# Kernel optimization log

Measured on AMD Instinct MI355X. Metric: run time of the kernel, lower is better.

The kernel has to match this reference:

```python
import jax, jax.numpy as jnp
import numpy as np
import math

B, S, D = 4, 2048, 1024
H, DK, DV = 16, 64, 64

def setup_inputs() -> dict:
    key = jax.random.key(0)
    ks = jax.random.split(key, 8)
    query = jax.random.normal(ks[0], (B, S, D), dtype=jnp.float32)
    key_t = jax.random.normal(ks[1], (B, S, D), dtype=jnp.float32)
    value = jax.random.normal(ks[2], (B, S, D), dtype=jnp.float32)
    # causal mask: True = masked (filled with -inf), broadcast over [B,H,S,S]
    mask = jnp.triu(jnp.ones((S, S), dtype=bool), k=1)[None, None, :, :]
    s = 0.02
    w_q = jax.random.normal(ks[3], (D, H * DK), dtype=jnp.float32) * s
    w_k = jax.random.normal(ks[4], (D, H * DK), dtype=jnp.float32) * s
    w_v = jax.random.normal(ks[5], (D, H * DV), dtype=jnp.float32) * s
    w_o = jax.random.normal(ks[6], (H * DV, D), dtype=jnp.float32) * s
    return {"query": query, "key": key_t, "value": value, "mask": mask,
            "w_q": w_q, "w_k": w_k, "w_v": w_v, "w_o": w_o}

def reference(query, key, value, mask, w_q, w_k, w_v, w_o):
    b, s, _ = query.shape
    # projections -> [B, H, S, dk/dv]
    q = (query @ w_q).reshape(b, s, H, DK).transpose(0, 2, 1, 3)
    k = (key @ w_k).reshape(b, s, H, DK).transpose(0, 2, 1, 3)
    v = (value @ w_v).reshape(b, s, H, DV).transpose(0, 2, 1, 3)
    scores = jnp.einsum('bhqd,bhkd->bhqk', q, k) / math.sqrt(DK)
    scores = jnp.where(mask, -jnp.inf, scores)
    attn = jax.nn.softmax(scores, axis=-1)
    out = jnp.einsum('bhqk,bhkd->bhqd', attn, v)
    out = out.transpose(0, 2, 1, 3).reshape(b, s, H * DV)
    return out @ w_o
```

## Files before the change

### kernel.cpp

```cpp
#include <hip/hip_runtime.h>
#include <hip/hip_bf16.h>

#define S_LEN 2048
#define NH 16
#define DHEAD 64
#define DMODEL 1024
#define BATCH 4

typedef __attribute__((ext_vector_type(4))) float f32x4;
typedef __attribute__((ext_vector_type(8))) short bf16x8;
typedef __attribute__((ext_vector_type(4))) short s16x4;
typedef __attribute__((ext_vector_type(4))) float fl4;
typedef __attribute__((ext_vector_type(4))) unsigned u32x4;
typedef __attribute__((ext_vector_type(2))) unsigned u32x2;

static __device__ __forceinline__ short f2bf(float f) {
  unsigned u = __builtin_bit_cast(unsigned, f);
  u += 0x7fffu + ((u >> 16) & 1u);
  return (short)(u >> 16);
}
static __device__ __forceinline__ f32x4 mfma16(bf16x8 a, bf16x8 b, f32x4 c) {
  return __builtin_amdgcn_mfma_f32_16x16x32_bf16(a, b, c, 0, 0, 0);
}
static __device__ __forceinline__ void gl_lds16(const short* g, short* l) {
  __builtin_amdgcn_global_load_lds(
      (const __attribute__((address_space(1))) unsigned*)g,
      (__attribute__((address_space(3))) unsigned*)l, 16, 0, 0);
}
static __device__ __forceinline__ unsigned cvt_pk_bf16(float lo, float hi) {
  unsigned r;
  asm("v_cvt_pk_bf16_f32 %0, %1, %2" : "=v"(r) : "v"(lo), "v"(hi));
  return r;
}

__global__ __launch_bounds__(256) void transpose_w3(
    const float* __restrict__ w0, const float* __restrict__ w1,
    const float* __restrict__ w2, short* __restrict__ o0,
    short* __restrict__ o1, short* __restrict__ o2) {
  const float* W = blockIdx.z == 0 ? w0 : blockIdx.z == 1 ? w1 : w2;
  short* O = blockIdx.z == 0 ? o0 : blockIdx.z == 1 ? o1 : o2;
  __shared__ __align__(16) short T[64][72];
  const int tid = threadIdx.x;
  const int k0 = blockIdx.y * 64, n0 = blockIdx.x * 64;
#pragma unroll
  for (int i = 0; i < 4; ++i) {
    int c = tid + i * 256;
    int kk = c >> 4, nn = (c & 15) << 2;
    fl4 v = *(const fl4*)(W + (size_t)(k0 + kk) * DMODEL + n0 + nn);
    T[nn + 0][kk] = f2bf(v.x);
    T[nn + 1][kk] = f2bf(v.y);
    T[nn + 2][kk] = f2bf(v.z);
    T[nn + 3][kk] = f2bf(v.w);
  }
  __syncthreads();
#pragma unroll
  for (int i = 0; i < 4; ++i) {
    int c = tid + i * 256;
    int nn = c >> 4, kk = (c & 15) << 2;
    *(s16x4*)(O + (size_t)(n0 + nn) * DMODEL + k0 + kk) = *(const s16x4*)&T[nn][kk];
  }
}

__global__ __launch_bounds__(256) void transpose_w1(
    const float* __restrict__ W, short* __restrict__ O) {
  __shared__ __align__(16) short T[64][72];
  const int tid = threadIdx.x;
  const int k0 = blockIdx.y * 64, n0 = blockIdx.x * 64;
#pragma unroll
  for (int i = 0; i < 4; ++i) {
    int c = tid + i * 256;
    int kk = c >> 4, nn = (c & 15) << 2;
    fl4 v = *(const fl4*)(W + (size_t)(k0 + kk) * DMODEL + n0 + nn);
    T[nn + 0][kk] = f2bf(v.x);
    T[nn + 1][kk] = f2bf(v.y);
    T[nn + 2][kk] = f2bf(v.z);
    T[nn + 3][kk] = f2bf(v.w);
  }
  __syncthreads();
#pragma unroll
  for (int i = 0; i < 4; ++i) {
    int c = tid + i * 256;
    int nn = c >> 4, kk = (c & 15) << 2;
    *(s16x4*)(O + (size_t)(n0 + nn) * DMODEL + k0 + kk) = *(const s16x4*)&T[nn][kk];
  }
}

__global__ __launch_bounds__(256) void gemm_qkv(
    const float* __restrict__ q, const float* __restrict__ k,
    const float* __restrict__ v, const short* __restrict__ Wtq,
    const short* __restrict__ Wtk, const short* __restrict__ Wtv,
    short* __restrict__ Qp, short* __restrict__ Kp, short* __restrict__ Vt,
    float qscale) {
  __shared__ __align__(16) short As[128 * 64];
  __shared__ __align__(16) short Bs[128 * 64];
  const int id = blockIdx.x;
  const int z = id >> 9;
  const int l = id & 511;
  const int cx = l & 7, j = l >> 3;
  const int n0 = (j & 7) * 128;
  const int m0 = (cx * 8 + (j >> 3)) * 128;

  const float* Af = z == 0 ? q : z == 1 ? k : v;
  const short* Bt = z == 0 ? Wtq : z == 1 ? Wtk : Wtv;
  short* Out = z == 0 ? Qp : z == 1 ? Kp : Vt;
  const float scale = z == 0 ? qscale : 1.0f;

  const int tid = threadIdx.x, lane = tid & 63, wid = tid >> 6;
  const int wm = (wid >> 1) * 64, wn = (wid & 1) * 64;
  const int lr = lane & 15, g = lane >> 4;

  f32x4 acc[4][4] = {};

  const int baseRow = tid >> 3;
  const int colOff = (((tid & 7) ^ (baseRow & 7)) << 3);
  const int slot0 = g ^ (lr & 7);

  fl4 av[8];
#pragma unroll
  for (int i = 0; i < 8; ++i) {
    const int c = tid + i * 256;
    av[i] = *(const fl4*)(Af + (size_t)(m0 + (c >> 4)) * DMODEL + ((c & 15) << 2));
  }

  for (int k0 = 0; k0 < DMODEL; k0 += 64) {
    __syncthreads();
#pragma unroll
    for (int i = 0; i < 8; ++i) {
      const int c = tid + i * 256;
      const int row = c >> 4, colc = c & 15;
      u32x2 pk;
      pk.x = cvt_pk_bf16(av[i].x, av[i].y);
      pk.y = cvt_pk_bf16(av[i].z, av[i].w);
      *(u32x2*)&As[row * 64 + (((colc >> 1) ^ (row & 7)) << 3) + ((colc & 1) << 2)] = pk;
    }
#pragma unroll
    for (int i = 0; i < 4; ++i) {
      const short* gb = Bt + (size_t)(n0 + baseRow + i * 32) * DMODEL + k0 + colOff;
      gl_lds16(gb, Bs + (tid + i * 256) * 8);
    }
    __syncthreads();

    if (k0 + 64 < DMODEL) {
#pragma unroll
      for (int i = 0; i < 8; ++i) {
        const int c = tid + i * 256;
        av[i] = *(const fl4*)(Af + (size_t)(m0 + (c >> 4)) * DMODEL + k0 + 64 + ((c & 15) << 2));
      }
    }

#pragma unroll
    for (int ks = 0; ks < 2; ++ks) {
      const int so = (slot0 ^ (ks << 2)) << 3;
      bf16x8 af[4], bfr[4];
#pragma unroll
      for (int t = 0; t < 4; ++t) {
        af[t] = *(const bf16x8*)&As[(wm + t * 16 + lr) * 64 + so];
        bfr[t] = *(const bf16x8*)&Bs[(wn + t * 16 + lr) * 64 + so];
      }
#pragma unroll
      for (int mi = 0; mi < 4; ++mi)
#pragma unroll
        for (int ni = 0; ni < 4; ++ni)
          acc[mi][ni] = mfma16(af[mi], bfr[ni], acc[mi][ni]);
    }
  }

  if (z < 2) {
#pragma unroll
    for (int mi = 0; mi < 4; ++mi)
#pragma unroll
      for (int ni = 0; ni < 4; ++ni) {
        const int n = n0 + wn + ni * 16 + lr;
        const int h = n >> 6, d = n & 63;
#pragma unroll
        for (int r = 0; r < 4; ++r) {
          const int m = m0 + wm + mi * 16 + g * 4 + r;
          const int b = m >> 11, s = m & (S_LEN - 1);
          Out[(((size_t)b * NH + h) * S_LEN + s) * DHEAD + d] =
              f2bf(acc[mi][ni][r] * scale);
        }
      }
  } else {
#pragma unroll
    for (int mi = 0; mi < 4; ++mi) {
      const int mb = m0 + wm + mi * 16 + g * 4;
      const int b = mb >> 11, s = mb & (S_LEN - 1);
#pragma unroll
      for (int ni = 0; ni < 4; ++ni) {
        const int n = n0 + wn + ni * 16 + lr;
        const int h = n >> 6, d = n & 63;
        s16x4 pv;
        pv.x = f2bf(acc[mi][ni][0]);
        pv.y = f2bf(acc[mi][ni][1]);
        pv.z = f2bf(acc[mi][ni][2]);
        pv.w = f2bf(acc[mi][ni][3]);
        *(s16x4*)(Out + (((size_t)b * NH + h) * DHEAD + d) * S_LEN + s) = pv;
      }
    }
  }
}

__global__ __launch_bounds__(256) void gemm_out(
    const short* __restrict__ Ab, const short* __restrict__ Bt,
    float* __restrict__ Out) {
  __shared__ __align__(16) short As[128 * 64];
  __shared__ __align__(16) short Bs[128 * 64];
  const int id = blockIdx.x;
  const int cx = id & 7, j = id >> 3;
  const int n0 = (j & 7) * 128;
  const int m0 = (cx * 8 + (j >> 3)) * 128;

  const int tid = threadIdx.x, lane = tid & 63, wid = tid >> 6;
  const int wm = (wid >> 1) * 64, wn = (wid & 1) * 64;
  const int lr = lane & 15, g = lane >> 4;

  f32x4 acc[4][4] = {};

  const int baseRow = tid >> 3;
  const int colOff = (((tid & 7) ^ (baseRow & 7)) << 3);
  const int slot0 = g ^ (lr & 7);

  for (int k0 = 0; k0 < DMODEL; k0 += 64) {
    __syncthreads();
#pragma unroll
    for (int i = 0; i < 4; ++i) {
      const short* ga = Ab + (size_t)(m0 + baseRow + i * 32) * DMODEL + k0 + colOff;
      gl_lds16(ga, As + (tid + i * 256) * 8);
      const short* gb = Bt + (size_t)(n0 + baseRow + i * 32) * DMODEL + k0 + colOff;
      gl_lds16(gb, Bs + (tid + i * 256) * 8);
    }
    __syncthreads();

#pragma unroll
    for (int ks = 0; ks < 2; ++ks) {
      const int so = (slot0 ^ (ks << 2)) << 3;
      bf16x8 af[4], bfr[4];
#pragma unroll
      for (int t = 0; t < 4; ++t) {
        af[t] = *(const bf16x8*)&As[(wm + t * 16 + lr) * 64 + so];
        bfr[t] = *(const bf16x8*)&Bs[(wn + t * 16 + lr) * 64 + so];
      }
#pragma unroll
      for (int mi = 0; mi < 4; ++mi)
#pragma unroll
        for (int ni = 0; ni < 4; ++ni)
          acc[mi][ni] = mfma16(af[mi], bfr[ni], acc[mi][ni]);
    }
  }

#pragma unroll
  for (int mi = 0; mi < 4; ++mi)
#pragma unroll
    for (int ni = 0; ni < 4; ++ni) {
      const int n = n0 + wn + ni * 16 + lr;
#pragma unroll
      for (int r = 0; r < 4; ++r) {
        const int m = m0 + wm + mi * 16 + g * 4 + r;
        Out[(size_t)m * DMODEL + n] = acc[mi][ni][r];
      }
    }
}

static __device__ __forceinline__ void softmax_pf_static(
    f32x4 (&st)[4], bf16x8& pf0, bf16x8& pf1) {
#pragma unroll
  for (int nj = 0; nj < 4; ++nj)
#pragma unroll
    for (int r = 0; r < 4; ++r)
      st[nj][r] = exp2f(st[nj][r]);
  unsigned pw[2][4];
#pragma unroll
  for (int kc = 0; kc < 2; ++kc)
#pragma unroll
    for (int jj = 0; jj < 2; ++jj) {
      unsigned a = cvt_pk_bf16(st[2 * kc][2 * jj], st[2 * kc][2 * jj + 1]);
      unsigned bb = cvt_pk_bf16(st[2 * kc + 1][2 * jj], st[2 * kc + 1][2 * jj + 1]);
      asm("v_permlane32_swap_b32 %0, %1" : "+v"(a), "+v"(bb));
      asm("v_permlane16_swap_b32 %0, %1" : "+v"(a), "+v"(bb));
      pw[kc][jj] = a;
      pw[kc][jj + 2] = bb;
    }
  u32x4 w0 = {pw[0][0], pw[0][1], pw[0][2], pw[0][3]};
  u32x4 w1 = {pw[1][0], pw[1][1], pw[1][2], pw[1][3]};
  pf0 = __builtin_bit_cast(bf16x8, w0);
  pf1 = __builtin_bit_cast(bf16x8, w1);
}

static __device__ __forceinline__ void attn_epilogue(
    f32x4 (&ot)[4], float lsum, int b, int h, int qa, int g,
    short* __restrict__ AO) {
  const float inv = 1.f / lsum;
  short* dst = AO + ((size_t)b * S_LEN + qa) * DMODEL + h * DHEAD + (g << 2);
#pragma unroll
  for (int nd = 0; nd < 4; ++nd) {
    s16x4 pv;
    pv.x = f2bf(ot[nd][0] * inv);
    pv.y = f2bf(ot[nd][1] * inv);
    pv.z = f2bf(ot[nd][2] * inv);
    pv.w = f2bf(ot[nd][3] * inv);
    *(s16x4*)(dst + nd * 16) = pv;
  }
}

__global__ __launch_bounds__(256) void attn9(
    const short* __restrict__ Qp, const short* __restrict__ Kp,
    const short* __restrict__ VT, short* __restrict__ AO) {
  __shared__ __align__(16) short KV[2][8192];
  const int tid = threadIdx.x, lane = tid & 63, wid = tid >> 6;
  const int lr = lane & 15, g = lane >> 4;
  const int id = blockIdx.x;
  const int xcd = id & 7;
  const int bh = xcd * 8 + ((id >> 3) & 7);
  const int sg = 31 - (id >> 6);
  const int t = sg * 4 + wid;
  const short* Qb = Qp + (size_t)bh * S_LEN * DHEAD;
  const short* Kb = Kp + (size_t)bh * S_LEN * DHEAD;
  const short* Vb = VT + (size_t)bh * DHEAD * S_LEN;
  const int b = bh >> 4, h = bh & 15;

  const int NT = sg + 1;
  const int q0 = t << 4;
  const int qa = q0 + lr;

  const int row1 = tid >> 3;
  const int col1 = (tid & 7) ^ (row1 & 7);
  const int kOff1 = row1 * DHEAD + col1 * 8;
  const int vOff1 = row1 * S_LEN + col1 * 8;

#define STAGE9(bufi, kvv) do {                                      \
    const short* ks_ = Kb + (size_t)(kvv) * DHEAD + kOff1;          \
    gl_lds16(ks_,               &KV[bufi][0] + tid * 8);            \
    gl_lds16(ks_ + 32 * DHEAD,  &KV[bufi][2048] + tid * 8);         \
    const short* vs_ = Vb + (kvv) + vOff1;                          \
    gl_lds16(vs_,               &KV[bufi][4096] + tid * 8);         \
    gl_lds16(vs_ + 32 * S_LEN,  &KV[bufi][6144] + tid * 8);         \
  } while (0)

  const int slot0 = g ^ (lr & 7);
  const int fOff0 = lr * 64 + slot0 * 8;
  const int fOff1 = lr * 64 + (slot0 ^ 4) * 8;

  bf16x8 qf[2];
  qf[0] = *(const bf16x8*)(Qb + (size_t)qa * DHEAD + (g << 3));
  qf[1] = *(const bf16x8*)(Qb + (size_t)qa * DHEAD + 32 + (g << 3));

  bf16x8 ones;
#pragma unroll
  for (int i = 0; i < 8; ++i) ones[i] = (short)0x3F80;

  f32x4 ot[4] = {};
  f32x4 lacc = {};

  STAGE9(0, 0);

  for (int it = 0; it < NT; ++it) {
    const int kv0 = it << 6;
    const int cb = it & 1;
    if (it + 1 < NT) {
      STAGE9(cb ^ 1, kv0 + 64);
      asm volatile("s_waitcnt vmcnt(4)" ::: "memory");
    } else {
      asm volatile("s_waitcnt vmcnt(0)" ::: "memory");
    }
    __builtin_amdgcn_s_barrier();

    const short* kb = &KV[cb][0];
    const short* vb = &KV[cb][4096];

    f32x4 st[4] = {};
    __builtin_amdgcn_s_setprio(1);
#pragma unroll
    for (int nj = 0; nj < 4; ++nj) {
      bf16x8 k0 = *(const bf16x8*)(kb + fOff0 + nj * 1024);
      bf16x8 k1 = *(const bf16x8*)(kb + fOff1 + nj * 1024);
      st[nj] = mfma16(k0, qf[0], st[nj]);
      st[nj] = mfma16(k1, qf[1], st[nj]);
    }
    __builtin_amdgcn_s_setprio(0);
    if (it == NT - 1) {
#pragma unroll
      for (int nj = 0; nj < 4; ++nj)
#pragma unroll
        for (int r = 0; r < 4; ++r)
          if (kv0 + nj * 16 + (g << 2) + r > qa) st[nj][r] = -1e30f;
    }
    bf16x8 pf0, pf1;
    softmax_pf_static(st, pf0, pf1);
    __builtin_amdgcn_s_setprio(1);
    lacc = mfma16(ones, pf0, lacc);
    lacc = mfma16(ones, pf1, lacc);
#pragma unroll
    for (int nd = 0; nd < 4; ++nd) {
      bf16x8 v0 = *(const bf16x8*)(vb + fOff0 + nd * 1024);
      bf16x8 v1 = *(const bf16x8*)(vb + fOff1 + nd * 1024);
      ot[nd] = mfma16(v0, pf0, ot[nd]);
      ot[nd] = mfma16(v1, pf1, ot[nd]);
    }
    __builtin_amdgcn_s_setprio(0);
    __builtin_amdgcn_s_barrier();
  }
#undef STAGE9

  attn_epilogue(ot, lacc[0], b, h, qa, g, AO);
}

extern "C" void kernel_launch(void* const* d_in, const int* in_sizes, int n_in,
                              void* d_out, int out_size, void* d_ws, size_t ws_size,
                              hipStream_t stream) {
  const float* query = (const float*)d_in[0];
  const float* key   = (const float*)d_in[1];
  const float* value = (const float*)d_in[2];
  const float* w_q = (const float*)d_in[4];
  const float* w_k = (const float*)d_in[5];
  const float* w_v = (const float*)d_in[6];
  const float* w_o = (const float*)d_in[7];

  const size_t QKV = (size_t)BATCH * NH * S_LEN * DHEAD;
  short* Qp = (short*)d_ws;
  short* Kp = Qp + QKV;
  short* Vt = Kp + QKV;
  short* AO = Vt + QKV;
  short* Wto = Qp;
  short* Wtq = (short*)d_out;
  short* Wtk = Wtq + (size_t)DMODEL * DMODEL;
  short* Wtv = Wtk + (size_t)DMODEL * DMODEL;

  dim3 blk(256);
  const float qscale = 0.125f * 1.4426950408889634f;

  transpose_w3<<<dim3(16, 16, 3), blk, 0, stream>>>(w_q, w_k, w_v, Wtq, Wtk, Wtv);
  gemm_qkv<<<dim3(1536), blk, 0, stream>>>(
      query, key, value, Wtq, Wtk, Wtv, Qp, Kp, Vt, qscale);
  attn9<<<dim3(2048), blk, 0, stream>>>(Qp, Kp, Vt, AO);
  transpose_w1<<<dim3(16, 16), blk, 0, stream>>>(w_o, Wto);
  gemm_out<<<dim3(512), blk, 0, stream>>>(AO, Wto, (float*)d_out);
}
```

Measured before the change: 178.5 us.

## Double-buffer LDS tiles in QKV projection GEMM with register-staged prefetch

Measured after the change: 172.9 us, median of 3. -3.1%, faster.

```diff
diff --git a/kernel.cpp b/kernel.cpp
--- a/kernel.cpp
+++ b/kernel.cpp
@@ -91,8 +91,8 @@
     const short* __restrict__ Wtk, const short* __restrict__ Wtv,
     short* __restrict__ Qp, short* __restrict__ Kp, short* __restrict__ Vt,
     float qscale) {
-  __shared__ __align__(16) short As[128 * 64];
-  __shared__ __align__(16) short Bs[128 * 64];
+  __shared__ __align__(16) short As[2][128 * 64];
+  __shared__ __align__(16) short Bs[2][128 * 64];
   const int id = blockIdx.x;
   const int z = id >> 9;
   const int l = id & 511;
@@ -115,47 +115,55 @@
   const int colOff = (((tid & 7) ^ (baseRow & 7)) << 3);
   const int slot0 = g ^ (lr & 7);
 
-  fl4 av[8];
-#pragma unroll
-  for (int i = 0; i < 8; ++i) {
-    const int c = tid + i * 256;
-    av[i] = *(const fl4*)(Af + (size_t)(m0 + (c >> 4)) * DMODEL + ((c & 15) << 2));
-  }
-
-  for (int k0 = 0; k0 < DMODEL; k0 += 64) {
-    __syncthreads();
-#pragma unroll
-    for (int i = 0; i < 8; ++i) {
-      const int c = tid + i * 256;
-      const int row = c >> 4, colc = c & 15;
-      u32x2 pk;
-      pk.x = cvt_pk_bf16(av[i].x, av[i].y);
-      pk.y = cvt_pk_bf16(av[i].z, av[i].w);
-      *(u32x2*)&As[row * 64 + (((colc >> 1) ^ (row & 7)) << 3) + ((colc & 1) << 2)] = pk;
-    }
-#pragma unroll
-    for (int i = 0; i < 4; ++i) {
-      const short* gb = Bt + (size_t)(n0 + baseRow + i * 32) * DMODEL + k0 + colOff;
-      gl_lds16(gb, Bs + (tid + i * 256) * 8);
-    }
-    __syncthreads();
-
-    if (k0 + 64 < DMODEL) {
-#pragma unroll
-      for (int i = 0; i < 8; ++i) {
-        const int c = tid + i * 256;
-        av[i] = *(const fl4*)(Af + (size_t)(m0 + (c >> 4)) * DMODEL + k0 + 64 + ((c & 15) << 2));
-      }
-    }
-
+  fl4 avA[8];
+  bf16x8 bvB[4];
+
+#define LOADS(kk0) do {                                                      \
+    _Pragma("unroll")                                                        \
+    for (int i = 0; i < 8; ++i) {                                            \
+      const int c = tid + i * 256;                                           \
+      avA[i] = *(const fl4*)(Af + (size_t)(m0 + (c >> 4)) * DMODEL + (kk0) + \
+                             ((c & 15) << 2));                               \
+    }                                                                        \
+    _Pragma("unroll")                                                        \
+    for (int i = 0; i < 4; ++i)                                              \
+      bvB[i] = *(const bf16x8*)(Bt + (size_t)(n0 + baseRow + i * 32) * DMODEL\
+                                + (kk0) + colOff);                           \
+  } while (0)
+
+#define WRITES(bufi) do {                                                    \
+    _Pragma("unroll")                                                        \
+    for (int i = 0; i < 8; ++i) {                                            \
+      const int c = tid + i * 256;                                           \
+      const int row = c >> 4, colc = c & 15;                                 \
+      u32x2 pk;                                                              \
+      pk.x = cvt_pk_bf16(avA[i].x, avA[i].y);                                \
+      pk.y = cvt_pk_bf16(avA[i].z, avA[i].w);                                \
+      *(u32x2*)&As[bufi][row * 64 + (((colc >> 1) ^ (row & 7)) << 3) +       \
+                         ((colc & 1) << 2)] = pk;                            \
+    }                                                                        \
+    _Pragma("unroll")                                                        \
+    for (int i = 0; i < 4; ++i)                                              \
+      *(bf16x8*)&Bs[bufi][(tid + i * 256) * 8] = bvB[i];                     \
+  } while (0)
+
+  LOADS(0);
+  asm volatile("s_waitcnt vmcnt(0)" ::: "memory");
+  WRITES(0);
+  LOADS(64);
+  asm volatile("s_waitcnt lgkmcnt(0)" ::: "memory");
+  __builtin_amdgcn_s_barrier();
+
+  for (int it = 0; it < 16; ++it) {
+    const int cb = it & 1;
 #pragma unroll
     for (int ks = 0; ks < 2; ++ks) {
       const int so = (slot0 ^ (ks << 2)) << 3;
       bf16x8 af[4], bfr[4];
 #pragma unroll
       for (int t = 0; t < 4; ++t) {
-        af[t] = *(const bf16x8*)&As[(wm + t * 16 + lr) * 64 + so];
-        bfr[t] = *(const bf16x8*)&Bs[(wn + t * 16 + lr) * 64 + so];
+        af[t] = *(const bf16x8*)&As[cb][(wm + t * 16 + lr) * 64 + so];
+        bfr[t] = *(const bf16x8*)&Bs[cb][(wn + t * 16 + lr) * 64 + so];
       }
 #pragma unroll
       for (int mi = 0; mi < 4; ++mi)
@@ -163,7 +171,19 @@
         for (int ni = 0; ni < 4; ++ni)
           acc[mi][ni] = mfma16(af[mi], bfr[ni], acc[mi][ni]);
     }
-  }
+    if (it < 15) {
+      asm volatile("s_waitcnt vmcnt(0)" ::: "memory");
+      WRITES(cb ^ 1);
+      if (it < 14) {
+        const int knext = (it + 2) * 64;
+        LOADS(knext);
+      }
+      asm volatile("s_waitcnt lgkmcnt(0)" ::: "memory");
+      __builtin_amdgcn_s_barrier();
+    }
+  }
+#undef LOADS
+#undef WRITES
 
   if (z < 2) {
 #pragma unroll
```
